# Performance work log

Hardware: AMD Instinct MI355X
Metric: run time of the kernel (lower is better)

Reference implementation:

```python
import jax, jax.numpy as jnp
import numpy as np


def setup_inputs() -> dict:
    key = jax.random.key(0)
    ks = jax.random.split(key, 7)
    B, T, E, H = 4, 4096, 1024, 64
    return {
        "idx": jax.random.normal(ks[0], (B, T, E), dtype=jnp.float32),
        "Wq": jax.random.normal(ks[1], (E, H), dtype=jnp.float32) * (E ** -0.5),
        "bq": jax.random.normal(ks[2], (H,), dtype=jnp.float32) * 0.01,
        "Wk": jax.random.normal(ks[3], (E, H), dtype=jnp.float32) * (E ** -0.5),
        "bk": jax.random.normal(ks[4], (H,), dtype=jnp.float32) * 0.01,
        "Wv": jax.random.normal(ks[5], (E, H), dtype=jnp.float32) * (E ** -0.5),
        "bv": jax.random.normal(ks[6], (H,), dtype=jnp.float32) * 0.01,
    }


def reference(idx, Wq, bq, Wk, bk, Wv, bv):
    # idx: [B, T, E]
    d = idx.shape[-1]  # note: torch code scales by n_embd**-0.5, NOT head_size
    Q = idx @ Wq + bq  # [B, T, H]
    K = idx @ Wk + bk
    V = idx @ Wv + bv
    # scores; NOTE: original torch code calls wei.masked_fill(...) non-in-place
    # and discards the result, so no causal mask is applied. No softmax either.
    wei = jnp.einsum("bth,bsh->bts", Q, K) * (d ** -0.5)  # [B, T, T]
    out = jnp.einsum("bts,bsh->bth", wei, V)  # [B, T, H]
    return out
```

## Files before the change

### kernel.cpp

```cpp
#include <hip/hip_runtime.h>


typedef __attribute__((ext_vector_type(8))) short bf16x8;
typedef __attribute__((ext_vector_type(4))) float f32x4;

#define MFMA16(a, b, c) __builtin_amdgcn_mfma_f32_16x16x32_bf16((a), (b), (c), 0, 0, 0)

__device__ __forceinline__ unsigned short f2bf(float f) {
    unsigned int u = __float_as_uint(f);
    u += 0x7fffu + ((u >> 16) & 1u);
    return (unsigned short)(u >> 16);
}

__global__ void prep(const float* __restrict__ Wq, const float* __restrict__ Wk,
                     const float* __restrict__ Wv, unsigned short* __restrict__ WB) {
    int t = blockIdx.x * 256 + threadIdx.x;
    int k0i = t / 768;
    int rem = t - k0i * 768;
    int nt = rem >> 6, lane = rem & 63;
    int n = nt * 16 + (lane & 15);
    int kb = k0i * 32 + ((lane >> 4) * 8);
    int mm = n >> 6, h = n & 63;
    const float* W = (mm == 0) ? Wq : (mm == 1) ? Wk : Wv;
    float sc = (mm == 1) ? 0.03125f : 1.0f;
    bf16x8 v;
    #pragma unroll
    for (int j = 0; j < 8; j++) v[j] = (short)f2bf(W[(size_t)(kb + j) * 64 + h] * sc);
    *(bf16x8*)(WB + (size_t)t * 8) = v;
}

__global__ __launch_bounds__(256, 2) void qkv(
    const float* __restrict__ idx, const unsigned short* __restrict__ WB,
    const float* __restrict__ bq, const float* __restrict__ bk, const float* __restrict__ bv,
    unsigned short* __restrict__ Q, unsigned short* __restrict__ Kt,
    unsigned short* __restrict__ Vt) {
    __shared__ float red[2][64][97];
    const int lane = threadIdx.x & 63, kh = threadIdx.x >> 6;
    const int r0 = blockIdx.x * 32;

    const float* aLoP = idx + (size_t)(r0 + (lane & 15)) * 1024 + kh * 256 + ((lane >> 4) * 8);
    const float* aHiP = aLoP + 16 * 1024;

    const f32x4 z4 = {0.f, 0.f, 0.f, 0.f};
    f32x4 accLo[12], accHi[12];
    #pragma unroll
    for (int i = 0; i < 12; i++) { accLo[i] = z4; accHi[i] = z4; }

    float4 c0 = *(const float4*)(aLoP);
    float4 c1 = *(const float4*)(aLoP + 4);
    float4 c2 = *(const float4*)(aHiP);
    float4 c3 = *(const float4*)(aHiP + 4);

    #pragma unroll 2
    for (int i = 0; i < 8; i++) {
        float4 n0 = c0, n1 = c1, n2 = c2, n3 = c3;
        if (i < 7) {
            n0 = *(const float4*)(aLoP + (i + 1) * 32);
            n1 = *(const float4*)(aLoP + (i + 1) * 32 + 4);
            n2 = *(const float4*)(aHiP + (i + 1) * 32);
            n3 = *(const float4*)(aHiP + (i + 1) * 32 + 4);
        }
        const unsigned short* Bp = WB + (size_t)(((kh * 8 + i) * 12) * 64 + lane) * 8;
        bf16x8 bb[12];
        #pragma unroll
        for (int nt = 0; nt < 12; nt++) bb[nt] = *(const bf16x8*)(Bp + nt * 512);
        bf16x8 aL, aH;
        aL[0] = (short)f2bf(c0.x); aL[1] = (short)f2bf(c0.y);
        aL[2] = (short)f2bf(c0.z); aL[3] = (short)f2bf(c0.w);
        aL[4] = (short)f2bf(c1.x); aL[5] = (short)f2bf(c1.y);
        aL[6] = (short)f2bf(c1.z); aL[7] = (short)f2bf(c1.w);
        aH[0] = (short)f2bf(c2.x); aH[1] = (short)f2bf(c2.y);
        aH[2] = (short)f2bf(c2.z); aH[3] = (short)f2bf(c2.w);
        aH[4] = (short)f2bf(c3.x); aH[5] = (short)f2bf(c3.y);
        aH[6] = (short)f2bf(c3.z); aH[7] = (short)f2bf(c3.w);
        #pragma unroll
        for (int nt = 0; nt < 12; nt++) {
            accLo[nt] = MFMA16(aL, bb[nt], accLo[nt]);
            accHi[nt] = MFMA16(aH, bb[nt], accHi[nt]);
        }
        c0 = n0; c1 = n1; c2 = n2; c3 = n3;
    }

    if (kh >= 2) {
        int buf = kh - 2;
        #pragma unroll
        for (int nt = 0; nt < 12; nt++)
            #pragma unroll
            for (int reg = 0; reg < 4; reg++) {
                red[buf][lane][nt * 4 + reg]      = accLo[nt][reg];
                red[buf][lane][48 + nt * 4 + reg] = accHi[nt][reg];
            }
    }
    __syncthreads();
    if (kh < 2) {
        #pragma unroll
        for (int nt = 0; nt < 12; nt++)
            #pragma unroll
            for (int reg = 0; reg < 4; reg++) {
                accLo[nt][reg] += red[kh][lane][nt * 4 + reg];
                accHi[nt][reg] += red[kh][lane][48 + nt * 4 + reg];
            }
    }
    __syncthreads();
    if (kh == 1) {
        #pragma unroll
        for (int nt = 0; nt < 12; nt++)
            #pragma unroll
            for (int reg = 0; reg < 4; reg++) {
                red[0][lane][nt * 4 + reg]      = accLo[nt][reg];
                red[0][lane][48 + nt * 4 + reg] = accHi[nt][reg];
            }
    }
    __syncthreads();
    if (kh == 0) {
        #pragma unroll
        for (int nt = 0; nt < 12; nt++) {
            int m = nt >> 2;
            int h = (nt & 3) * 16 + (lane & 15);
            float bias = (m == 0) ? bq[h] : (m == 1) ? bk[h] * 0.03125f : bv[h];
            #pragma unroll
            for (int rg = 0; rg < 2; rg++) {
                int rbase = r0 + rg * 16 + (lane >> 4) * 4;
                #pragma unroll
                for (int reg = 0; reg < 4; reg++) {
                    float s = (rg ? accHi[nt][reg] : accLo[nt][reg])
                              + red[0][lane][rg * 48 + nt * 4 + reg] + bias;
                    int r = rbase + reg;
                    unsigned short v = f2bf(s);
                    if (m == 0) {
                        Q[(size_t)r * 64 + h] = v;
                    } else {
                        int b = r >> 12, t = r & 4095;
                        unsigned short* dst = (m == 1) ? Kt : Vt;
                        dst[(size_t)b * 262144 + h * 4096 + t] = v;
                    }
                }
            }
        }
    }
}

__global__ __launch_bounds__(256) void ktv_partial(
    const unsigned short* __restrict__ Kt, const unsigned short* __restrict__ Vt,
    float* __restrict__ part) {
    const int lane = threadIdx.x & 63, wave = threadIdx.x >> 6;
    const int c = blockIdx.x, b = blockIdx.y;
    const unsigned short* Kb = Kt + (size_t)b * 262144;
    const unsigned short* Vb = Vt + (size_t)b * 262144;
    const f32x4 z4 = {0.f, 0.f, 0.f, 0.f};
    f32x4 acc[4] = {z4, z4, z4, z4};
    const int m  = 16 * wave + (lane & 15);
    const int tq = (lane >> 4) * 8;
    #pragma unroll
    for (int it = 0; it < 8; it++) {
        int t0 = c * 256 + it * 32 + tq;
        bf16x8 a = *(const bf16x8*)&Kb[(size_t)m * 4096 + t0];
        #pragma unroll
        for (int nt = 0; nt < 4; nt++) {
            bf16x8 bb = *(const bf16x8*)&Vb[(size_t)(nt * 16 + (lane & 15)) * 4096 + t0];
            acc[nt] = MFMA16(a, bb, acc[nt]);
        }
    }
    float* P = part + (size_t)(b * 16 + c) * 4096;
    const int rowb = 16 * wave + (lane >> 4) * 4;
    #pragma unroll
    for (int nt = 0; nt < 4; nt++)
        #pragma unroll
        for (int reg = 0; reg < 4; reg++)
            P[(rowb + reg) * 64 + nt * 16 + (lane & 15)] = acc[nt][reg];
}

__global__ void reduce_m(const float* __restrict__ part,
                         unsigned short* __restrict__ Mt) {
    int i = blockIdx.x * 256 + threadIdx.x;
    int b = i >> 12, h1 = (i >> 6) & 63, h2 = i & 63;
    float s = 0.f;
    #pragma unroll
    for (int cc = 0; cc < 16; cc++)
        s += part[(size_t)(b * 16 + cc) * 4096 + h1 * 64 + h2];
    Mt[(size_t)b * 4096 + h2 * 64 + h1] = f2bf(s);
}

__global__ __launch_bounds__(256) void qm(
    const unsigned short* __restrict__ Q, const unsigned short* __restrict__ Mt,
    float* __restrict__ out) {
    const int lane = threadIdx.x & 63, wave = threadIdx.x >> 6;
    const int r0 = blockIdx.x * 64;
    const int b  = r0 >> 12;
    const f32x4 z4 = {0.f, 0.f, 0.f, 0.f};
    f32x4 acc[4] = {z4, z4, z4, z4};
    const int rr = r0 + 16 * wave + (lane & 15);
    const int kq = (lane >> 4) * 8;
    #pragma unroll
    for (int ks = 0; ks < 2; ks++) {
        int k0 = ks * 32;
        bf16x8 a = *(const bf16x8*)&Q[(size_t)rr * 64 + k0 + kq];
        #pragma unroll
        for (int nt = 0; nt < 4; nt++) {
            bf16x8 bb = *(const bf16x8*)&Mt[(size_t)b * 4096 + (nt * 16 + (lane & 15)) * 64 + k0 + kq];
            acc[nt] = MFMA16(a, bb, acc[nt]);
        }
    }
    const int rowb = r0 + 16 * wave + (lane >> 4) * 4;
    #pragma unroll
    for (int nt = 0; nt < 4; nt++)
        #pragma unroll
        for (int reg = 0; reg < 4; reg++)
            out[(size_t)(rowb + reg) * 64 + nt * 16 + (lane & 15)] = acc[nt][reg];
}

extern "C" void kernel_launch(void* const* d_in, const int* in_sizes, int n_in,
                              void* d_out, int out_size, void* d_ws, size_t ws_size,
                              hipStream_t stream) {
    const float* idx = (const float*)d_in[0];
    const float* Wq  = (const float*)d_in[1];
    const float* bq  = (const float*)d_in[2];
    const float* Wk  = (const float*)d_in[3];
    const float* bk  = (const float*)d_in[4];
    const float* Wv  = (const float*)d_in[5];
    const float* bv  = (const float*)d_in[6];
    float* out = (float*)d_out;

    char* ws = (char*)d_ws;
    unsigned short* WB = (unsigned short*)(ws);
    float*          Pp = (float*)(ws);
    unsigned short* Q  = (unsigned short*)(ws + (1024u << 10));
    unsigned short* Kt = (unsigned short*)(ws + (3072u << 10));
    unsigned short* Vt = (unsigned short*)(ws + (5120u << 10));
    unsigned short* Mt = (unsigned short*)(ws + (7168u << 10));

    hipLaunchKernelGGL(prep,        dim3(96),     dim3(256), 0, stream, Wq, Wk, Wv, WB);
    hipLaunchKernelGGL(qkv,         dim3(512),    dim3(256), 0, stream,
                       idx, WB, bq, bk, bv, Q, Kt, Vt);
    hipLaunchKernelGGL(ktv_partial, dim3(16, 4),  dim3(256), 0, stream, Kt, Vt, Pp);
    hipLaunchKernelGGL(reduce_m,    dim3(64),     dim3(256), 0, stream, Pp, Mt);
    hipLaunchKernelGGL(qm,          dim3(256),    dim3(256), 0, stream, Q, Mt, out);
}
```

Baseline: 133.2 us.

## Halve rows per QKV block, preload A fragments, and split K^T V finer

The QKV projection kernel now handles 16 rows per block instead of 32 and doubles the grid to 1024 blocks. It loads and converts the whole A slice to bf16 up front rather than double-buffering it, and raises the occupancy hint to 3 blocks per CU. The K^T V partial kernel is split into 32 chunks per batch instead of 16, and the reduction and workspace offsets are adjusted to match. The aim is more parallelism and latency hiding on the memory-bound projection, at the cost of loading each weight fragment for only half as many rows and doubling the partial-sum traffic.

```diff
diff --git a/kernel.cpp b/kernel.cpp
--- a/kernel.cpp
+++ b/kernel.cpp
@@ -29,87 +29,72 @@
     *(bf16x8*)(WB + (size_t)t * 8) = v;
 }
 
-__global__ __launch_bounds__(256, 2) void qkv(
+__global__ __launch_bounds__(256, 3) void qkv(
     const float* __restrict__ idx, const unsigned short* __restrict__ WB,
     const float* __restrict__ bq, const float* __restrict__ bk, const float* __restrict__ bv,
     unsigned short* __restrict__ Q, unsigned short* __restrict__ Kt,
     unsigned short* __restrict__ Vt) {
-    __shared__ float red[2][64][97];
+    __shared__ float red[2][64][49];
     const int lane = threadIdx.x & 63, kh = threadIdx.x >> 6;
-    const int r0 = blockIdx.x * 32;
-
-    const float* aLoP = idx + (size_t)(r0 + (lane & 15)) * 1024 + kh * 256 + ((lane >> 4) * 8);
-    const float* aHiP = aLoP + 16 * 1024;
+    const int r0 = blockIdx.x * 16;
+
+    const float* aP = idx + (size_t)(r0 + (lane & 15)) * 1024 + kh * 256 + ((lane >> 4) * 8);
+
+    float4 af[16];
+    #pragma unroll
+    for (int it = 0; it < 8; it++) {
+        af[it * 2]     = *(const float4*)(aP + it * 32);
+        af[it * 2 + 1] = *(const float4*)(aP + it * 32 + 4);
+    }
+    bf16x8 aF[8];
+    #pragma unroll
+    for (int it = 0; it < 8; it++) {
+        float4 lo = af[it * 2], hi = af[it * 2 + 1];
+        bf16x8 a;
+        a[0] = (short)f2bf(lo.x); a[1] = (short)f2bf(lo.y);
+        a[2] = (short)f2bf(lo.z); a[3] = (short)f2bf(lo.w);
+        a[4] = (short)f2bf(hi.x); a[5] = (short)f2bf(hi.y);
+        a[6] = (short)f2bf(hi.z); a[7] = (short)f2bf(hi.w);
+        aF[it] = a;
+    }
 
     const f32x4 z4 = {0.f, 0.f, 0.f, 0.f};
-    f32x4 accLo[12], accHi[12];
-    #pragma unroll
-    for (int i = 0; i < 12; i++) { accLo[i] = z4; accHi[i] = z4; }
-
-    float4 c0 = *(const float4*)(aLoP);
-    float4 c1 = *(const float4*)(aLoP + 4);
-    float4 c2 = *(const float4*)(aHiP);
-    float4 c3 = *(const float4*)(aHiP + 4);
-
-    #pragma unroll 2
+    f32x4 acc[12];
+    #pragma unroll
+    for (int i = 0; i < 12; i++) acc[i] = z4;
+
+    #pragma unroll
     for (int i = 0; i < 8; i++) {
-        float4 n0 = c0, n1 = c1, n2 = c2, n3 = c3;
-        if (i < 7) {
-            n0 = *(const float4*)(aLoP + (i + 1) * 32);
-            n1 = *(const float4*)(aLoP + (i + 1) * 32 + 4);
-            n2 = *(const float4*)(aHiP + (i + 1) * 32);
-            n3 = *(const float4*)(aHiP + (i + 1) * 32 + 4);
-        }
         const unsigned short* Bp = WB + (size_t)(((kh * 8 + i) * 12) * 64 + lane) * 8;
-        bf16x8 bb[12];
-        #pragma unroll
-        for (int nt = 0; nt < 12; nt++) bb[nt] = *(const bf16x8*)(Bp + nt * 512);
-        bf16x8 aL, aH;
-        aL[0] = (short)f2bf(c0.x); aL[1] = (short)f2bf(c0.y);
-        aL[2] = (short)f2bf(c0.z); aL[3] = (short)f2bf(c0.w);
-        aL[4] = (short)f2bf(c1.x); aL[5] = (short)f2bf(c1.y);
-        aL[6] = (short)f2bf(c1.z); aL[7] = (short)f2bf(c1.w);
-        aH[0] = (short)f2bf(c2.x); aH[1] = (short)f2bf(c2.y);
-        aH[2] = (short)f2bf(c2.z); aH[3] = (short)f2bf(c2.w);
-        aH[4] = (short)f2bf(c3.x); aH[5] = (short)f2bf(c3.y);
-        aH[6] = (short)f2bf(c3.z); aH[7] = (short)f2bf(c3.w);
         #pragma unroll
         for (int nt = 0; nt < 12; nt++) {
-            accLo[nt] = MFMA16(aL, bb[nt], accLo[nt]);
-            accHi[nt] = MFMA16(aH, bb[nt], accHi[nt]);
-        }
-        c0 = n0; c1 = n1; c2 = n2; c3 = n3;
+            bf16x8 bb = *(const bf16x8*)(Bp + nt * 512);
+            acc[nt] = MFMA16(aF[i], bb, acc[nt]);
+        }
     }
 
     if (kh >= 2) {
-        int buf = kh - 2;
         #pragma unroll
         for (int nt = 0; nt < 12; nt++)
             #pragma unroll
-            for (int reg = 0; reg < 4; reg++) {
-                red[buf][lane][nt * 4 + reg]      = accLo[nt][reg];
-                red[buf][lane][48 + nt * 4 + reg] = accHi[nt][reg];
-            }
+            for (int reg = 0; reg < 4; reg++)
+                red[kh - 2][lane][nt * 4 + reg] = acc[nt][reg];
     }
     __syncthreads();
     if (kh < 2) {
         #pragma unroll
         for (int nt = 0; nt < 12; nt++)
             #pragma unroll
-            for (int reg = 0; reg < 4; reg++) {
-                accLo[nt][reg] += red[kh][lane][nt * 4 + reg];
-                accHi[nt][reg] += red[kh][lane][48 + nt * 4 + reg];
-            }
+            for (int reg = 0; reg < 4; reg++)
+                acc[nt][reg] += red[kh][lane][nt * 4 + reg];
     }
     __syncthreads();
     if (kh == 1) {
         #pragma unroll
         for (int nt = 0; nt < 12; nt++)
             #pragma unroll
-            for (int reg = 0; reg < 4; reg++) {
-                red[0][lane][nt * 4 + reg]      = accLo[nt][reg];
-                red[0][lane][48 + nt * 4 + reg] = accHi[nt][reg];
-            }
+            for (int reg = 0; reg < 4; reg++)
+                red[0][lane][nt * 4 + reg] = acc[nt][reg];
     }
     __syncthreads();
     if (kh == 0) {
@@ -118,22 +103,18 @@
             int m = nt >> 2;
             int h = (nt & 3) * 16 + (lane & 15);
             float bias = (m == 0) ? bq[h] : (m == 1) ? bk[h] * 0.03125f : bv[h];
-            #pragma unroll
-            for (int rg = 0; rg < 2; rg++) {
-                int rbase = r0 + rg * 16 + (lane >> 4) * 4;
-                #pragma unroll
-                for (int reg = 0; reg < 4; reg++) {
-                    float s = (rg ? accHi[nt][reg] : accLo[nt][reg])
-                              + red[0][lane][rg * 48 + nt * 4 + reg] + bias;
-                    int r = rbase + reg;
-                    unsigned short v = f2bf(s);
-                    if (m == 0) {
-                        Q[(size_t)r * 64 + h] = v;
-                    } else {
-                        int b = r >> 12, t = r & 4095;
-                        unsigned short* dst = (m == 1) ? Kt : Vt;
-                        dst[(size_t)b * 262144 + h * 4096 + t] = v;
-                    }
+            int rbase = r0 + (lane >> 4) * 4;
+            #pragma unroll
+            for (int reg = 0; reg < 4; reg++) {
+                float s = acc[nt][reg] + red[0][lane][nt * 4 + reg] + bias;
+                int r = rbase + reg;
+                unsigned short v = f2bf(s);
+                if (m == 0) {
+                    Q[(size_t)r * 64 + h] = v;
+                } else {
+                    int b = r >> 12, t = r & 4095;
+                    unsigned short* dst = (m == 1) ? Kt : Vt;
+                    dst[(size_t)b * 262144 + h * 4096 + t] = v;
                 }
             }
         }
@@ -152,8 +133,8 @@
     const int m  = 16 * wave + (lane & 15);
     const int tq = (lane >> 4) * 8;
     #pragma unroll
-    for (int it = 0; it < 8; it++) {
-        int t0 = c * 256 + it * 32 + tq;
+    for (int it = 0; it < 4; it++) {
+        int t0 = c * 128 + it * 32 + tq;
         bf16x8 a = *(const bf16x8*)&Kb[(size_t)m * 4096 + t0];
         #pragma unroll
         for (int nt = 0; nt < 4; nt++) {
@@ -161,7 +142,7 @@
             acc[nt] = MFMA16(a, bb, acc[nt]);
         }
     }
-    float* P = part + (size_t)(b * 16 + c) * 4096;
+    float* P = part + (size_t)(b * 32 + c) * 4096;
     const int rowb = 16 * wave + (lane >> 4) * 4;
     #pragma unroll
     for (int nt = 0; nt < 4; nt++)
@@ -176,8 +157,8 @@
     int b = i >> 12, h1 = (i >> 6) & 63, h2 = i & 63;
     float s = 0.f;
     #pragma unroll
-    for (int cc = 0; cc < 16; cc++)
-        s += part[(size_t)(b * 16 + cc) * 4096 + h1 * 64 + h2];
+    for (int cc = 0; cc < 32; cc++)
+        s += part[(size_t)(b * 32 + cc) * 4096 + h1 * 64 + h2];
     Mt[(size_t)b * 4096 + h2 * 64 + h1] = f2bf(s);
 }
 
@@ -224,15 +205,15 @@
     char* ws = (char*)d_ws;
     unsigned short* WB = (unsigned short*)(ws);
     float*          Pp = (float*)(ws);
-    unsigned short* Q  = (unsigned short*)(ws + (1024u << 10));
-    unsigned short* Kt = (unsigned short*)(ws + (3072u << 10));
-    unsigned short* Vt = (unsigned short*)(ws + (5120u << 10));
-    unsigned short* Mt = (unsigned short*)(ws + (7168u << 10));
+    unsigned short* Q  = (unsigned short*)(ws + (2048u << 10));
+    unsigned short* Kt = (unsigned short*)(ws + (4096u << 10));
+    unsigned short* Vt = (unsigned short*)(ws + (6144u << 10));
+    unsigned short* Mt = (unsigned short*)(ws + (8192u << 10));
 
     hipLaunchKernelGGL(prep,        dim3(96),     dim3(256), 0, stream, Wq, Wk, Wv, WB);
-    hipLaunchKernelGGL(qkv,         dim3(512),    dim3(256), 0, stream,
+    hipLaunchKernelGGL(qkv,         dim3(1024),   dim3(256), 0, stream,
                        idx, WB, bq, bk, bv, Q, Kt, Vt);
-    hipLaunchKernelGGL(ktv_partial, dim3(16, 4),  dim3(256), 0, stream, Kt, Vt, Pp);
+    hipLaunchKernelGGL(ktv_partial, dim3(32, 4),  dim3(256), 0, stream, Kt, Vt, Pp);
     hipLaunchKernelGGL(reduce_m,    dim3(64),     dim3(256), 0, stream, Pp, Mt);
     hipLaunchKernelGGL(qm,          dim3(256),    dim3(256), 0, stream, Q, Mt, out);
 }
```

After: 138.2 us. +3.7%, slower.
